# Performance work log

Hardware: AMD Instinct MI355X
Metric: run time of the kernel (lower is better)

The kernel has to match this reference:

```python
import jax, jax.numpy as jnp
import numpy as np

N_NODE = 200000
EMB = 64
N_EDGES = 2000000
LAYERS = 3
EPS_NORM = 1e-12


def setup_inputs() -> dict:
    key = jax.random.key(0)
    ks = jax.random.split(key, 13)
    d = EMB
    return {
        "user_emb": jax.random.normal(ks[0], (N_NODE, d), jnp.float32),
        "W0": jax.random.normal(ks[1], (d, d), jnp.float32) * np.float32(np.sqrt(2.0 / d)),
        "b0": jax.random.normal(ks[2], (1, d), jnp.float32) * 0.1,
        "W1": jax.random.normal(ks[3], (d, d), jnp.float32) * np.float32(np.sqrt(2.0 / d)),
        "b1": jax.random.normal(ks[4], (1, d), jnp.float32) * 0.1,
        "att": jax.random.normal(ks[5], (1, d), jnp.float32) * 0.1,
        "att_m": jax.random.normal(ks[6], (d, d), jnp.float32) * np.float32(np.sqrt(2.0 / d)),
        "item_rows": jax.random.randint(ks[7], (N_EDGES,), 0, N_NODE, jnp.int32),
        "item_cols": jax.random.randint(ks[8], (N_EDGES,), 0, N_NODE, jnp.int32),
        "item_vals": jax.random.uniform(ks[9], (N_EDGES,), jnp.float32),
        "user_rows": jax.random.randint(ks[10], (N_EDGES,), 0, N_NODE, jnp.int32),
        "user_cols": jax.random.randint(ks[11], (N_EDGES,), 0, N_NODE, jnp.int32),
        "user_vals": jax.random.uniform(ks[12], (N_EDGES,), jnp.float32),
    }


def _spmm(rows, cols, vals, x):
    # y[i] = sum_{edges (i,j)} vals * x[j]   (torch.sparse.mm equivalent)
    gathered = vals[:, None] * x[cols]  # [E, d]
    return jax.ops.segment_sum(gathered, rows, num_segments=N_NODE)


def _l2norm_rows(x):
    # F.normalize(x, p=2, dim=1)
    n = jnp.sqrt(jnp.sum(x * x, axis=1, keepdims=True))
    return x / jnp.maximum(n, EPS_NORM)


def _self_gating(em, W, b):
    return em * jax.nn.sigmoid(em @ W + b)


def _propagate(rows, cols, vals, u):
    acc = u
    for _ in range(LAYERS):
        u = _spmm(rows, cols, vals, u)
        acc = acc + _l2norm_rows(u)
    return acc


def reference(user_emb, W0, b0, W1, b1, att, att_m,
              item_rows, item_cols, item_vals,
              user_rows, user_cols, user_vals):
    u_c2 = _self_gating(user_emb, W0, b0)
    u_c3 = _self_gating(user_emb, W1, b1)
    e2 = _propagate(item_rows, item_cols, item_vals, u_c2)  # [N, d]
    e3 = _propagate(user_rows, user_cols, user_vals, u_c3)  # [N, d]
    # channel attention: per-node scalar score for each channel
    w2 = jnp.sum(att * (e2 @ att_m), axis=1)  # [N]
    w3 = jnp.sum(att * (e3 @ att_m), axis=1)  # [N]
    score = jax.nn.softmax(jnp.stack([w2, w3], axis=1), axis=-1)  # [N, 2]
    mixed = score[:, 0:1] * e2 + score[:, 1:2] * e3  # [N, d]
    return mixed, score
```

## Files before the change

kernel.cpp:

```cpp
#include <hip/hip_runtime.h>

#define N_NODE 200000
#define EMB 64
#define N_EDGES 2000000
#define NROWS_TOTAL (2 * N_NODE)
#define TOT_E (2 * N_EDGES)

#define BSHIFT 9
#define BROWS 512
#define NBUCK ((NROWS_TOTAL + BROWS - 1) / BROWS)
#define NB 1024
#define CHUNK ((TOT_E + NB - 1) / NB)
#define SCAN_N (NBUCK * NB)
#define MAXH 6144

typedef unsigned short bfu;
typedef __attribute__((ext_vector_type(8))) short bf16x8;
typedef __attribute__((ext_vector_type(4))) float f32x4;

__device__ __forceinline__ float bf2f(bfu u) { return __uint_as_float(((unsigned)u) << 16); }
__device__ __forceinline__ bfu f2bf(float f) {
    unsigned b = __float_as_uint(f);
    return (bfu)((b + 0x7FFF + ((b >> 16) & 1)) >> 16);
}
__device__ __forceinline__ unsigned packcv(int col, float v) {
    int q = (int)(v * 16384.0f + 0.5f);
    q = q < 0 ? 0 : (q > 16383 ? 16383 : q);
    return ((unsigned)col << 14) | (unsigned)q;
}

__global__ void gate_kernel(const float* __restrict__ emb,
                            const float* __restrict__ W,
                            const float* __restrict__ b,
                            bfu* __restrict__ out, int n) {
    int t = threadIdx.x;
    int w = t >> 6, lane = t & 63;
    int l16 = lane & 15, kg = lane >> 4;
    bf16x8 Bf[2][4];
#pragma unroll
    for (int kb = 0; kb < 2; ++kb)
#pragma unroll
        for (int nt = 0; nt < 4; ++nt) {
            bf16x8 f;
#pragma unroll
            for (int e = 0; e < 8; ++e)
                f[e] = (short)f2bf(W[(kb * 32 + kg * 8 + e) * 64 + nt * 16 + l16]);
            Bf[kb][nt] = f;
        }
    float bias[4];
#pragma unroll
    for (int nt = 0; nt < 4; ++nt) bias[nt] = b[nt * 16 + l16];
    const float4* e4 = (const float4*)emb;
#pragma unroll 1
    for (int it = 0; it < 4; ++it) {
        int tile = blockIdx.x * 16 + w * 4 + it;
        if (tile * 16 >= n) break;
        int arow = tile * 16 + l16;
        size_t ab = (size_t)arow * 16 + kg * 2;
        float4 a0 = e4[ab], a1 = e4[ab + 1];
        float4 a2 = e4[ab + 8], a3 = e4[ab + 9];
        bf16x8 A0, A1;
        A0[0] = (short)f2bf(a0.x); A0[1] = (short)f2bf(a0.y);
        A0[2] = (short)f2bf(a0.z); A0[3] = (short)f2bf(a0.w);
        A0[4] = (short)f2bf(a1.x); A0[5] = (short)f2bf(a1.y);
        A0[6] = (short)f2bf(a1.z); A0[7] = (short)f2bf(a1.w);
        A1[0] = (short)f2bf(a2.x); A1[1] = (short)f2bf(a2.y);
        A1[2] = (short)f2bf(a2.z); A1[3] = (short)f2bf(a2.w);
        A1[4] = (short)f2bf(a3.x); A1[5] = (short)f2bf(a3.y);
        A1[6] = (short)f2bf(a3.z); A1[7] = (short)f2bf(a3.w);
        f32x4 acc[4];
#pragma unroll
        for (int nt = 0; nt < 4; ++nt) {
            acc[nt] = (f32x4){0.f, 0.f, 0.f, 0.f};
            acc[nt] = __builtin_amdgcn_mfma_f32_16x16x32_bf16(A0, Bf[0][nt], acc[nt], 0, 0, 0);
            acc[nt] = __builtin_amdgcn_mfma_f32_16x16x32_bf16(A1, Bf[1][nt], acc[nt], 0, 0, 0);
        }
#pragma unroll
        for (int nt = 0; nt < 4; ++nt) {
#pragma unroll
            for (int r = 0; r < 4; ++r) {
                int orow = tile * 16 + kg * 4 + r;
                int col = nt * 16 + l16;
                float s = acc[nt][r] + bias[nt];
                float g = 1.0f / (1.0f + __expf(-s));
                float xv = emb[(size_t)orow * 64 + col];
                out[(size_t)orow * 64 + col] = f2bf(xv * g);
            }
        }
    }
}

__global__ void binA_kernel(const int* __restrict__ item_rows,
                            const int* __restrict__ user_rows,
                            int* __restrict__ bc) {
    __shared__ int h[NBUCK];
    int t = threadIdx.x, blk = blockIdx.x;
    for (int k = t; k < NBUCK; k += 256) h[k] = 0;
    __syncthreads();
    int lo = blk * CHUNK, hi = min(lo + CHUNK, TOT_E);
    for (int i = lo + t; i < hi; i += 256) {
        int g = (i < N_EDGES) ? item_rows[i] : (N_NODE + user_rows[i - N_EDGES]);
        atomicAdd(&h[g >> BSHIFT], 1);
    }
    __syncthreads();
    for (int k = t; k < NBUCK; k += 256) bc[k * NB + blk] = h[k];
}

__global__ void scan1_kernel(const int* __restrict__ bc, int* __restrict__ bsumP,
                             int* __restrict__ btot) {
    int b = blockIdx.x, t = threadIdx.x;
    int base = b * NB + t * 4;
    int sR = 0, sP = 0;
#pragma unroll
    for (int k = 0; k < 4; ++k) {
        int c = bc[base + k];
        sR += c;
        sP += (c + 7) & ~7;
    }
#pragma unroll
    for (int off = 32; off; off >>= 1) {
        sR += __shfl_xor(sR, off);
        sP += __shfl_xor(sP, off);
    }
    __shared__ int wsR[4], wsP[4];
    int lane = t & 63, w = t >> 6;
    if (lane == 0) { wsR[w] = sR; wsP[w] = sP; }
    __syncthreads();
    if (t == 0) {
        btot[b] = wsR[0] + wsR[1] + wsR[2] + wsR[3];
        bsumP[b] = wsP[0] + wsP[1] + wsP[2] + wsP[3];
    }
}

__global__ void scan2_kernel(const int* __restrict__ bsumP, const int* __restrict__ btot,
                             int* __restrict__ boffP, int* __restrict__ bbase) {
    __shared__ int sh[1024];
    int t = threadIdx.x;
    int vP = (t < NBUCK) ? bsumP[t] : 0;
    sh[t] = vP;
    __syncthreads();
    for (int off = 1; off < 1024; off <<= 1) {
        int u = (t >= off) ? sh[t - off] : 0;
        __syncthreads();
        sh[t] += u;
        __syncthreads();
    }
    if (t < NBUCK) boffP[t] = sh[t] - vP;
    if (t == 1023) boffP[NBUCK] = sh[1023];
    __syncthreads();
    int vR = (t < NBUCK) ? btot[t] : 0;
    sh[t] = vR;
    __syncthreads();
    for (int off = 1; off < 1024; off <<= 1) {
        int u = (t >= off) ? sh[t - off] : 0;
        __syncthreads();
        sh[t] += u;
        __syncthreads();
    }
    if (t < NBUCK) bbase[t] = sh[t] - vR;
}

__global__ void scan3_kernel(const int* __restrict__ bc, const int* __restrict__ boffP,
                             int* __restrict__ soffP) {
    int b = blockIdx.x, t = threadIdx.x;
    int lane = t & 63, w = t >> 6;
    int base = b * NB + t * 4;
    int p[4];
#pragma unroll
    for (int k = 0; k < 4; ++k) p[k] = (bc[base + k] + 7) & ~7;
    int e1 = p[0], e2 = p[0] + p[1], e3 = p[0] + p[1] + p[2];
    int tsum = e3 + p[3];
    int incl = tsum;
#pragma unroll
    for (int off = 1; off < 64; off <<= 1) {
        int u = __shfl_up(incl, off);
        if (lane >= off) incl += u;
    }
    int excl = incl - tsum;
    __shared__ int wsum[4];
    if (lane == 63) wsum[w] = incl;
    __syncthreads();
    int woff = 0;
    for (int k = 0; k < 4; ++k) if (k < w) woff += wsum[k];
    int g = boffP[b] + woff + excl;
    soffP[base + 0] = g;
    soffP[base + 1] = g + e1;
    soffP[base + 2] = g + e2;
    soffP[base + 3] = g + e3;
}

__global__ void binB_kernel(const int* __restrict__ item_rows, const int* __restrict__ item_cols,
                            const float* __restrict__ item_vals,
                            const int* __restrict__ user_rows, const int* __restrict__ user_cols,
                            const float* __restrict__ user_vals,
                            const int* __restrict__ bc, const int* __restrict__ soffP,
                            int2* __restrict__ staged) {
    __shared__ int2 ebuf[CHUNK];
    __shared__ unsigned short sbk[CHUNK];
    __shared__ int lbase[NBUCK + 1];
    __shared__ int lcur[NBUCK];
    __shared__ int gb[NBUCK];
    __shared__ int wsum[4];
    int t = threadIdx.x, blk = blockIdx.x;
    for (int k = t; k < NBUCK; k += 256) gb[k] = soffP[k * NB + blk];
    {
        int i0 = t * 4;
        int p0 = (i0 < NBUCK) ? bc[i0 * NB + blk] : 0;
        int p1 = (i0 + 1 < NBUCK) ? bc[(i0 + 1) * NB + blk] : 0;
        int p2 = (i0 + 2 < NBUCK) ? bc[(i0 + 2) * NB + blk] : 0;
        int p3 = (i0 + 3 < NBUCK) ? bc[(i0 + 3) * NB + blk] : 0;
        int tsum = p0 + p1 + p2 + p3;
        int lane = t & 63, w = t >> 6;
        int incl = tsum;
#pragma unroll
        for (int off = 1; off < 64; off <<= 1) {
            int u = __shfl_up(incl, off);
            if (lane >= off) incl += u;
        }
        if (lane == 63) wsum[w] = incl;
        __syncthreads();
        int woff = 0;
        for (int k = 0; k < w; ++k) woff += wsum[k];
        int excl = woff + incl - tsum;
        if (i0 < NBUCK) { lbase[i0] = excl; lcur[i0] = excl; }
        if (i0 + 1 < NBUCK) { lbase[i0 + 1] = excl + p0; lcur[i0 + 1] = excl + p0; }
        if (i0 + 2 < NBUCK) { lbase[i0 + 2] = excl + p0 + p1; lcur[i0 + 2] = excl + p0 + p1; }
        if (i0 + 3 < NBUCK) { lbase[i0 + 3] = excl + p0 + p1 + p2; lcur[i0 + 3] = excl + p0 + p1 + p2; }
        if (t == 255) lbase[NBUCK] = excl + tsum;
    }
    __syncthreads();
    int lo = blk * CHUNK, hi = min(lo + CHUNK, TOT_E);
    int cnt = hi - lo;
    for (int i = lo + t; i < hi; i += 256) {
        int g, c; float v;
        if (i < N_EDGES) { g = item_rows[i]; c = item_cols[i]; v = item_vals[i]; }
        else { int j = i - N_EDGES; g = N_NODE + user_rows[j]; c = user_cols[j]; v = user_vals[j]; }
        int bk = g >> BSHIFT;
        int s = atomicAdd(&lcur[bk], 1);
        ebuf[s] = make_int2(((g & (BROWS - 1)) << 18) | c, __float_as_int(v));
        sbk[s] = (unsigned short)bk;
    }
    __syncthreads();
    for (int j = t; j < cnt; j += 256) {
        int k = sbk[j];
        staged[gb[k] + (j - lbase[k])] = ebuf[j];
    }
    for (int k = t; k < NBUCK; k += 256) {
        int c = lbase[k + 1] - lbase[k];
        int s = gb[k] + c, e = gb[k] + ((c + 7) & ~7);
        for (int q = s; q < e; ++q) staged[q] = make_int2(-1, 0);
    }
}

__global__ void finalize_kernel(const int2* __restrict__ staged, const int* __restrict__ boffP,
                                const int* __restrict__ bbase,
                                int* __restrict__ row_ptr, unsigned* __restrict__ ecv) {
    __shared__ int hist[BROWS];
    __shared__ int start[BROWS + 1];
    __shared__ int2 ebuf[MAXH];
    __shared__ int wsum[4];
    int b = blockIdx.x, t = threadIdx.x;
    int base = boffP[b], end = boffP[b + 1];
    int ebase = bbase[b];
    hist[t * 2] = 0; hist[t * 2 + 1] = 0;
    __syncthreads();
    for (int k = base + t; k < end; k += 256) {
        int gx = staged[k].x;
        if (gx >= 0) atomicAdd(&hist[gx >> 18], 1);
    }
    __syncthreads();
    int i0 = t * 2;
    int c0 = hist[i0], c1 = hist[i0 + 1];
    int tsum = c0 + c1;
    int lane = t & 63, w = t >> 6;
    int incl = tsum;
#pragma unroll
    for (int off = 1; off < 64; off <<= 1) {
        int u = __shfl_up(incl, off);
        if (lane >= off) incl += u;
    }
    if (lane == 63) wsum[w] = incl;
    __syncthreads();
    int woff = 0;
    for (int k = 0; k < w; ++k) woff += wsum[k];
    int excl = woff + incl - tsum;
    start[i0] = excl; start[i0 + 1] = excl + c0;
    if (t == 255) start[BROWS] = excl + tsum;
    __syncthreads();
    int tot = start[BROWS];
#pragma unroll
    for (int q = 0; q < 2; ++q) {
        int r = i0 + q;
        int g = (b << BSHIFT) + r;
        if (g < NROWS_TOTAL) row_ptr[g] = ebase + start[r];
    }
    if (b == 0 && t == 0) row_ptr[NROWS_TOTAL] = TOT_E;
    if (tot <= MAXH) {
        hist[i0] = start[i0]; hist[i0 + 1] = start[i0 + 1];
        __syncthreads();
        for (int k = base + t; k < end; k += 256) {
            int2 p = staged[k];
            if (p.x < 0) continue;
            int l = atomicAdd(&hist[p.x >> 18], 1);
            ebuf[l] = make_int2(p.x & 0x3FFFF, p.y);
        }
        __syncthreads();
        for (int j = t; j < tot; j += 256) {
            int2 q = ebuf[j];
            ecv[ebase + j] = packcv(q.x, __int_as_float(q.y));
        }
    } else {
        hist[i0] = ebase + start[i0]; hist[i0 + 1] = ebase + start[i0 + 1];
        __syncthreads();
        for (int k = base + t; k < end; k += 256) {
            int2 p = staged[k];
            if (p.x < 0) continue;
            int pos = atomicAdd(&hist[p.x >> 18], 1);
            ecv[pos] = packcv(p.x & 0x3FFFF, __int_as_float(p.y));
        }
    }
}

__global__ void spmm_y(const int* __restrict__ row_ptr, const unsigned* __restrict__ ecv,
                       const bfu* __restrict__ x,
                       bfu* __restrict__ y, float* __restrict__ rinv, int n) {
    int t = threadIdx.x;
    int lane = t & 63;
    int sub = lane >> 4;
    int l16 = lane & 15;
    int i = blockIdx.x * 16 + (t >> 6) * 4 + sub;
    if (i >= n) return;
    int s = row_ptr[i], e = row_ptr[i + 1];
    const ushort4* x4 = (const ushort4*)x;
    float4 a = make_float4(0.f, 0.f, 0.f, 0.f);
    int gbase = sub * 16;
    for (int base = s; base < e; base += 16) {
        int idx = base + l16;
        unsigned pl = 0;
        if (idx < e) pl = ecv[idx];
        int cnt = min(16, e - base);
        int cnt4 = (cnt + 3) & ~3;
        for (int k = 0; k < cnt4; k += 4) {
#pragma unroll
            for (int u = 0; u < 4; ++u) {
                unsigned p = (unsigned)__shfl((int)pl, gbase + k + u);
                int c = p >> 14;
                float v = (float)(p & 16383u) * (1.0f / 16384.0f);
                ushort4 xv = x4[(size_t)c * 16 + l16];
                a.x += v * bf2f(xv.x); a.y += v * bf2f(xv.y);
                a.z += v * bf2f(xv.z); a.w += v * bf2f(xv.w);
            }
        }
    }
    size_t o4 = (size_t)i * 16 + l16;
    ushort4 bv;
    bv.x = f2bf(a.x); bv.y = f2bf(a.y); bv.z = f2bf(a.z); bv.w = f2bf(a.w);
    ((ushort4*)y)[o4] = bv;
    float sq = a.x * a.x + a.y * a.y + a.z * a.z + a.w * a.w;
#pragma unroll
    for (int off = 8; off; off >>= 1) sq += __shfl_xor(sq, off);
    if (l16 == 0) rinv[i] = 1.0f / fmaxf(sqrtf(sq), 1e-12f);
}

__global__ void spmm_sum(const int* __restrict__ row_ptr, const unsigned* __restrict__ ecv,
                         const bfu* __restrict__ x ,
                         const bfu* __restrict__ u0, const bfu* __restrict__ y1,
                         const float* __restrict__ r1, const float* __restrict__ r2,
                         float* __restrict__ mixed, int n) {
    int t = threadIdx.x;
    int lane = t & 63;
    int sub = lane >> 4;
    int l16 = lane & 15;
    int i = blockIdx.x * 16 + (t >> 6) * 4 + sub;
    if (i >= n) return;
    int s = row_ptr[i], e = row_ptr[i + 1];
    const ushort4* x4 = (const ushort4*)x;
    float4 a = make_float4(0.f, 0.f, 0.f, 0.f);
    int gbase = sub * 16;
    for (int base = s; base < e; base += 16) {
        int idx = base + l16;
        unsigned pl = 0;
        if (idx < e) pl = ecv[idx];
        int cnt = min(16, e - base);
        int cnt4 = (cnt + 3) & ~3;
        for (int k = 0; k < cnt4; k += 4) {
#pragma unroll
            for (int u = 0; u < 4; ++u) {
                unsigned p = (unsigned)__shfl((int)pl, gbase + k + u);
                int c = p >> 14;
                float v = (float)(p & 16383u) * (1.0f / 16384.0f);
                ushort4 xv = x4[(size_t)c * 16 + l16];
                a.x += v * bf2f(xv.x); a.y += v * bf2f(xv.y);
                a.z += v * bf2f(xv.z); a.w += v * bf2f(xv.w);
            }
        }
    }
    float sq = a.x * a.x + a.y * a.y + a.z * a.z + a.w * a.w;
#pragma unroll
    for (int off = 8; off; off >>= 1) sq += __shfl_xor(sq, off);
    float r3 = 1.0f / fmaxf(sqrtf(sq), 1e-12f);
    size_t o4 = (size_t)i * 16 + l16;
    float a1 = r1[i], a2 = r2[i];
    ushort4 b0 = ((const ushort4*)u0)[o4];
    ushort4 b1 = ((const ushort4*)y1)[o4];
    ushort4 b2 = ((const ushort4*)x)[o4];
    float4 o;
    o.x = bf2f(b0.x) + a1 * bf2f(b1.x) + a2 * bf2f(b2.x) + r3 * a.x;
    o.y = bf2f(b0.y) + a1 * bf2f(b1.y) + a2 * bf2f(b2.y) + r3 * a.y;
    o.z = bf2f(b0.z) + a1 * bf2f(b1.z) + a2 * bf2f(b2.z) + r3 * a.z;
    o.w = bf2f(b0.w) + a1 * bf2f(b1.w) + a2 * bf2f(b2.w) + r3 * a.w;
    ((float4*)mixed)[o4] = o;
}

__global__ void spmm_mix(const int* __restrict__ row_ptr, const unsigned* __restrict__ ecv,
                         const bfu* __restrict__ x ,
                         const bfu* __restrict__ u0, const bfu* __restrict__ y1,
                         const float* __restrict__ r1, const float* __restrict__ r2,
                         float* __restrict__ mixed, const float* __restrict__ vvec,
                         float* __restrict__ score, int n) {
    int t = threadIdx.x;
    int lane = t & 63;
    int sub = lane >> 4;
    int l16 = lane & 15;
    int i = blockIdx.x * 16 + (t >> 6) * 4 + sub;
    if (i >= n) return;
    int s = row_ptr[i], e = row_ptr[i + 1];
    const ushort4* x4 = (const ushort4*)x;
    float4 a = make_float4(0.f, 0.f, 0.f, 0.f);
    int gbase = sub * 16;
    for (int base = s; base < e; base += 16) {
        int idx = base + l16;
        unsigned pl = 0;
        if (idx < e) pl = ecv[idx];
        int cnt = min(16, e - base);
        int cnt4 = (cnt + 3) & ~3;
        for (int k = 0; k < cnt4; k += 4) {
#pragma unroll
            for (int u = 0; u < 4; ++u) {
                unsigned p = (unsigned)__shfl((int)pl, gbase + k + u);
                int c = p >> 14;
                float v = (float)(p & 16383u) * (1.0f / 16384.0f);
                ushort4 xv = x4[(size_t)c * 16 + l16];
                a.x += v * bf2f(xv.x); a.y += v * bf2f(xv.y);
                a.z += v * bf2f(xv.z); a.w += v * bf2f(xv.w);
            }
        }
    }
    float sq = a.x * a.x + a.y * a.y + a.z * a.z + a.w * a.w;
#pragma unroll
    for (int off = 8; off; off >>= 1) sq += __shfl_xor(sq, off);
    float r3 = 1.0f / fmaxf(sqrtf(sq), 1e-12f);
    size_t o4 = (size_t)i * 16 + l16;
    float a1 = r1[i], a2s = r2[i];
    ushort4 b0 = ((const ushort4*)u0)[o4];
    ushort4 b1 = ((const ushort4*)y1)[o4];
    ushort4 b2 = ((const ushort4*)x)[o4];
    float4 a3;
    a3.x = bf2f(b0.x) + a1 * bf2f(b1.x) + a2s * bf2f(b2.x) + r3 * a.x;
    a3.y = bf2f(b0.y) + a1 * bf2f(b1.y) + a2s * bf2f(b2.y) + r3 * a.y;
    a3.z = bf2f(b0.z) + a1 * bf2f(b1.z) + a2s * bf2f(b2.z) + r3 * a.z;
    a3.w = bf2f(b0.w) + a1 * bf2f(b1.w) + a2s * bf2f(b2.w) + r3 * a.w;
    float4 a2 = ((float4*)mixed)[o4];
    float4 vv = ((const float4*)vvec)[l16];
    float w2 = a2.x * vv.x + a2.y * vv.y + a2.z * vv.z + a2.w * vv.w;
    float w3 = a3.x * vv.x + a3.y * vv.y + a3.z * vv.z + a3.w * vv.w;
#pragma unroll
    for (int off = 8; off; off >>= 1) {
        w2 += __shfl_xor(w2, off);
        w3 += __shfl_xor(w3, off);
    }
    float m = fmaxf(w2, w3);
    float x2 = __expf(w2 - m), x3 = __expf(w3 - m);
    float inv = 1.0f / (x2 + x3);
    float s2 = x2 * inv, s3 = x3 * inv;
    float4 o;
    o.x = s2 * a2.x + s3 * a3.x; o.y = s2 * a2.y + s3 * a3.y;
    o.z = s2 * a2.z + s3 * a3.z; o.w = s2 * a2.w + s3 * a3.w;
    ((float4*)mixed)[o4] = o;
    if (l16 == 0) { score[(size_t)i * 2] = s2; score[(size_t)i * 2 + 1] = s3; }
}

__global__ void vvec_kernel(const float* __restrict__ att_m, const float* __restrict__ att,
                            float* __restrict__ v) {
    int k = threadIdx.x;
    float s = 0.0f;
    for (int j = 0; j < 64; ++j) s += att_m[k * 64 + j] * att[j];
    v[k] = s;
}

extern "C" void kernel_launch(void* const* d_in, const int* in_sizes, int n_in,
                              void* d_out, int out_size, void* d_ws, size_t ws_size,
                              hipStream_t stream) {
    const float* user_emb = (const float*)d_in[0];
    const float* W0 = (const float*)d_in[1];
    const float* b0 = (const float*)d_in[2];
    const float* W1 = (const float*)d_in[3];
    const float* b1 = (const float*)d_in[4];
    const float* att = (const float*)d_in[5];
    const float* att_m = (const float*)d_in[6];
    const int* item_rows = (const int*)d_in[7];
    const int* item_cols = (const int*)d_in[8];
    const float* item_vals = (const float*)d_in[9];
    const int* user_rows = (const int*)d_in[10];
    const int* user_cols = (const int*)d_in[11];
    const float* user_vals = (const float*)d_in[12];

    float* out = (float*)d_out;
    float* mixed = out;
    float* score = out + (size_t)N_NODE * 64;

    char* w = (char*)d_ws;
    bfu* u0 = (bfu*)w;         w += (size_t)N_NODE * 64 * 2;
    bfu* y1 = (bfu*)w;         w += (size_t)N_NODE * 64 * 2;
    bfu* y2 = (bfu*)w;         w += (size_t)N_NODE * 64 * 2;
    float* rv1 = (float*)w;    w += (size_t)N_NODE * 4;
    float* rv2 = (float*)w;    w += (size_t)N_NODE * 4;
    int* row_ptr = (int*)w;    w += ((size_t)NROWS_TOTAL + 64) * 4;
    unsigned* ecv = (unsigned*)w; w += (size_t)TOT_E * 4;
    float* vvec = (float*)w;   w += 256;
    int* bc = (int*)w;         w += (size_t)SCAN_N * 4;
    int* soffP = (int*)w;      w += (size_t)SCAN_N * 4;
    int* bsumP = (int*)w;      w += (NBUCK + 8) * 4;
    int* btot = (int*)w;       w += (NBUCK + 8) * 4;
    int* boffP = (int*)w;      w += (NBUCK + 8) * 4;
    int* bbase = (int*)w;      w += (NBUCK + 8) * 4;
    int2* staged = (int2*)u0;

    const int NB16 = (N_NODE + 15) / 16;
    const int GATE_B = (N_NODE / 16 + 15) / 16;
    const int* rp_item = row_ptr;
    const int* rp_user = row_ptr + N_NODE;

    binA_kernel<<<NB, 256, 0, stream>>>(item_rows, user_rows, bc);
    scan1_kernel<<<NBUCK, 256, 0, stream>>>(bc, bsumP, btot);
    scan2_kernel<<<1, 1024, 0, stream>>>(bsumP, btot, boffP, bbase);
    scan3_kernel<<<NBUCK, 256, 0, stream>>>(bc, boffP, soffP);
    binB_kernel<<<NB, 256, 0, stream>>>(item_rows, item_cols, item_vals,
                                        user_rows, user_cols, user_vals, bc, soffP, staged);
    finalize_kernel<<<NBUCK, 256, 0, stream>>>(staged, boffP, bbase, row_ptr, ecv);
    vvec_kernel<<<1, 64, 0, stream>>>(att_m, att, vvec);

    gate_kernel<<<GATE_B, 256, 0, stream>>>(user_emb, W0, b0, u0, N_NODE);
    spmm_y<<<NB16, 256, 0, stream>>>(rp_item, ecv, u0, y1, rv1, N_NODE);
    spmm_y<<<NB16, 256, 0, stream>>>(rp_item, ecv, y1, y2, rv2, N_NODE);
    spmm_sum<<<NB16, 256, 0, stream>>>(rp_item, ecv, y2, u0, y1, rv1, rv2, mixed, N_NODE);

    gate_kernel<<<GATE_B, 256, 0, stream>>>(user_emb, W1, b1, u0, N_NODE);
    spmm_y<<<NB16, 256, 0, stream>>>(rp_user, ecv, u0, y1, rv1, N_NODE);
    spmm_y<<<NB16, 256, 0, stream>>>(rp_user, ecv, y1, y2, rv2, N_NODE);
    spmm_mix<<<NB16, 256, 0, stream>>>(rp_user, ecv, y2, u0, y1, rv1, rv2,
                                       mixed, vvec, score, N_NODE);
}
```

Before: 438.3 us.

## Batch both propagation channels into single launches over stacked node rows

Doubles the workspace buffers so the item and user channels are stored side by side. The two gating passes and the per-layer SpMMs for both channels each run as one launch over all rows, and the final layer of both channels is merged with the attention mix into a single kernel. This cuts the launch count, avoids writing then re-reading the intermediate mixed output, and gives each SpMM launch twice the rows to fill the GPU. In exchange the workspace footprint grows and the final kernel does two gathers per thread, which raises register pressure.

```diff
diff --git a/kernel.cpp b/kernel.cpp
--- a/kernel.cpp
+++ b/kernel.cpp
@@ -13,6 +13,7 @@
 #define CHUNK ((TOT_E + NB - 1) / NB)
 #define SCAN_N (NBUCK * NB)
 #define MAXH 6144
+#define GATE_B ((N_NODE / 16 + 15) / 16)
 
 typedef unsigned short bfu;
 typedef __attribute__((ext_vector_type(8))) short bf16x8;
@@ -29,10 +30,16 @@
     return ((unsigned)col << 14) | (unsigned)q;
 }
 
-__global__ void gate_kernel(const float* __restrict__ emb,
-                            const float* __restrict__ W,
-                            const float* __restrict__ b,
-                            bfu* __restrict__ out, int n) {
+__global__ void gate2_kernel(const float* __restrict__ emb,
+                             const float* __restrict__ W0, const float* __restrict__ b0,
+                             const float* __restrict__ W1, const float* __restrict__ b1,
+                             bfu* __restrict__ out) {
+    int blk = blockIdx.x;
+    int half = (blk >= GATE_B) ? 1 : 0;
+    const float* W = half ? W1 : W0;
+    const float* b = half ? b1 : b0;
+    bfu* o = out + (size_t)half * N_NODE * 64;
+    int bblk = blk - half * GATE_B;
     int t = threadIdx.x;
     int w = t >> 6, lane = t & 63;
     int l16 = lane & 15, kg = lane >> 4;
@@ -53,8 +60,8 @@
     const float4* e4 = (const float4*)emb;
 #pragma unroll 1
     for (int it = 0; it < 4; ++it) {
-        int tile = blockIdx.x * 16 + w * 4 + it;
-        if (tile * 16 >= n) break;
+        int tile = bblk * 16 + w * 4 + it;
+        if (tile * 16 >= N_NODE) break;
         int arow = tile * 16 + l16;
         size_t ab = (size_t)arow * 16 + kg * 2;
         float4 a0 = e4[ab], a1 = e4[ab + 1];
@@ -84,7 +91,7 @@
                 float s = acc[nt][r] + bias[nt];
                 float g = 1.0f / (1.0f + __expf(-s));
                 float xv = emb[(size_t)orow * 64 + col];
-                out[(size_t)orow * 64 + col] = f2bf(xv * g);
+                o[(size_t)orow * 64 + col] = f2bf(xv * g);
             }
         }
     }
@@ -323,13 +330,14 @@
 
 __global__ void spmm_y(const int* __restrict__ row_ptr, const unsigned* __restrict__ ecv,
                        const bfu* __restrict__ x,
-                       bfu* __restrict__ y, float* __restrict__ rinv, int n) {
+                       bfu* __restrict__ y, float* __restrict__ rinv) {
     int t = threadIdx.x;
     int lane = t & 63;
     int sub = lane >> 4;
     int l16 = lane & 15;
     int i = blockIdx.x * 16 + (t >> 6) * 4 + sub;
-    if (i >= n) return;
+    if (i >= NROWS_TOTAL) return;
+    size_t off16 = (i >= N_NODE) ? (size_t)N_NODE * 16 : 0;
     int s = row_ptr[i], e = row_ptr[i + 1];
     const ushort4* x4 = (const ushort4*)x;
     float4 a = make_float4(0.f, 0.f, 0.f, 0.f);
@@ -346,7 +354,7 @@
                 unsigned p = (unsigned)__shfl((int)pl, gbase + k + u);
                 int c = p >> 14;
                 float v = (float)(p & 16383u) * (1.0f / 16384.0f);
-                ushort4 xv = x4[(size_t)c * 16 + l16];
+                ushort4 xv = x4[(size_t)c * 16 + off16 + l16];
                 a.x += v * bf2f(xv.x); a.y += v * bf2f(xv.y);
                 a.z += v * bf2f(xv.z); a.w += v * bf2f(xv.w);
             }
@@ -362,108 +370,92 @@
     if (l16 == 0) rinv[i] = 1.0f / fmaxf(sqrtf(sq), 1e-12f);
 }
 
-__global__ void spmm_sum(const int* __restrict__ row_ptr, const unsigned* __restrict__ ecv,
-                         const bfu* __restrict__ x ,
+__global__ void spmm_fin(const int* __restrict__ row_ptr, const unsigned* __restrict__ ecv,
+                         const bfu* __restrict__ y2 ,
                          const bfu* __restrict__ u0, const bfu* __restrict__ y1,
-                         const float* __restrict__ r1, const float* __restrict__ r2,
-                         float* __restrict__ mixed, int n) {
+                         const float* __restrict__ rv1, const float* __restrict__ rv2,
+                         float* __restrict__ mixed, const float* __restrict__ vvec,
+                         float* __restrict__ score) {
     int t = threadIdx.x;
     int lane = t & 63;
     int sub = lane >> 4;
     int l16 = lane & 15;
     int i = blockIdx.x * 16 + (t >> 6) * 4 + sub;
-    if (i >= n) return;
-    int s = row_ptr[i], e = row_ptr[i + 1];
-    const ushort4* x4 = (const ushort4*)x;
-    float4 a = make_float4(0.f, 0.f, 0.f, 0.f);
+    if (i >= N_NODE) return;
+    const ushort4* x4 = (const ushort4*)y2;
     int gbase = sub * 16;
-    for (int base = s; base < e; base += 16) {
-        int idx = base + l16;
-        unsigned pl = 0;
-        if (idx < e) pl = ecv[idx];
-        int cnt = min(16, e - base);
-        int cnt4 = (cnt + 3) & ~3;
-        for (int k = 0; k < cnt4; k += 4) {
-#pragma unroll
-            for (int u = 0; u < 4; ++u) {
-                unsigned p = (unsigned)__shfl((int)pl, gbase + k + u);
-                int c = p >> 14;
-                float v = (float)(p & 16383u) * (1.0f / 16384.0f);
-                ushort4 xv = x4[(size_t)c * 16 + l16];
-                a.x += v * bf2f(xv.x); a.y += v * bf2f(xv.y);
-                a.z += v * bf2f(xv.z); a.w += v * bf2f(xv.w);
+    float4 a2v = make_float4(0.f, 0.f, 0.f, 0.f);
+    {
+        int s = row_ptr[i], e = row_ptr[i + 1];
+        for (int base = s; base < e; base += 16) {
+            int idx = base + l16;
+            unsigned pl = 0;
+            if (idx < e) pl = ecv[idx];
+            int cnt = min(16, e - base);
+            int cnt4 = (cnt + 3) & ~3;
+            for (int k = 0; k < cnt4; k += 4) {
+#pragma unroll
+                for (int u = 0; u < 4; ++u) {
+                    unsigned p = (unsigned)__shfl((int)pl, gbase + k + u);
+                    int c = p >> 14;
+                    float v = (float)(p & 16383u) * (1.0f / 16384.0f);
+                    ushort4 xv = x4[(size_t)c * 16 + l16];
+                    a2v.x += v * bf2f(xv.x); a2v.y += v * bf2f(xv.y);
+                    a2v.z += v * bf2f(xv.z); a2v.w += v * bf2f(xv.w);
+                }
             }
         }
     }
-    float sq = a.x * a.x + a.y * a.y + a.z * a.z + a.w * a.w;
-#pragma unroll
-    for (int off = 8; off; off >>= 1) sq += __shfl_xor(sq, off);
-    float r3 = 1.0f / fmaxf(sqrtf(sq), 1e-12f);
-    size_t o4 = (size_t)i * 16 + l16;
-    float a1 = r1[i], a2 = r2[i];
-    ushort4 b0 = ((const ushort4*)u0)[o4];
-    ushort4 b1 = ((const ushort4*)y1)[o4];
-    ushort4 b2 = ((const ushort4*)x)[o4];
-    float4 o;
-    o.x = bf2f(b0.x) + a1 * bf2f(b1.x) + a2 * bf2f(b2.x) + r3 * a.x;
-    o.y = bf2f(b0.y) + a1 * bf2f(b1.y) + a2 * bf2f(b2.y) + r3 * a.y;
-    o.z = bf2f(b0.z) + a1 * bf2f(b1.z) + a2 * bf2f(b2.z) + r3 * a.z;
-    o.w = bf2f(b0.w) + a1 * bf2f(b1.w) + a2 * bf2f(b2.w) + r3 * a.w;
-    ((float4*)mixed)[o4] = o;
-}
-
-__global__ void spmm_mix(const int* __restrict__ row_ptr, const unsigned* __restrict__ ecv,
-                         const bfu* __restrict__ x ,
-                         const bfu* __restrict__ u0, const bfu* __restrict__ y1,
-                         const float* __restrict__ r1, const float* __restrict__ r2,
-                         float* __restrict__ mixed, const float* __restrict__ vvec,
-                         float* __restrict__ score, int n) {
-    int t = threadIdx.x;
-    int lane = t & 63;
-    int sub = lane >> 4;
-    int l16 = lane & 15;
-    int i = blockIdx.x * 16 + (t >> 6) * 4 + sub;
-    if (i >= n) return;
-    int s = row_ptr[i], e = row_ptr[i + 1];
-    const ushort4* x4 = (const ushort4*)x;
-    float4 a = make_float4(0.f, 0.f, 0.f, 0.f);
-    int gbase = sub * 16;
-    for (int base = s; base < e; base += 16) {
-        int idx = base + l16;
-        unsigned pl = 0;
-        if (idx < e) pl = ecv[idx];
-        int cnt = min(16, e - base);
-        int cnt4 = (cnt + 3) & ~3;
-        for (int k = 0; k < cnt4; k += 4) {
-#pragma unroll
-            for (int u = 0; u < 4; ++u) {
-                unsigned p = (unsigned)__shfl((int)pl, gbase + k + u);
-                int c = p >> 14;
-                float v = (float)(p & 16383u) * (1.0f / 16384.0f);
-                ushort4 xv = x4[(size_t)c * 16 + l16];
-                a.x += v * bf2f(xv.x); a.y += v * bf2f(xv.y);
-                a.z += v * bf2f(xv.z); a.w += v * bf2f(xv.w);
+    float4 a3v = make_float4(0.f, 0.f, 0.f, 0.f);
+    {
+        int s = row_ptr[N_NODE + i], e = row_ptr[N_NODE + i + 1];
+        for (int base = s; base < e; base += 16) {
+            int idx = base + l16;
+            unsigned pl = 0;
+            if (idx < e) pl = ecv[idx];
+            int cnt = min(16, e - base);
+            int cnt4 = (cnt + 3) & ~3;
+            for (int k = 0; k < cnt4; k += 4) {
+#pragma unroll
+                for (int u = 0; u < 4; ++u) {
+                    unsigned p = (unsigned)__shfl((int)pl, gbase + k + u);
+                    int c = p >> 14;
+                    float v = (float)(p & 16383u) * (1.0f / 16384.0f);
+                    ushort4 xv = x4[(size_t)c * 16 + (size_t)N_NODE * 16 + l16];
+                    a3v.x += v * bf2f(xv.x); a3v.y += v * bf2f(xv.y);
+                    a3v.z += v * bf2f(xv.z); a3v.w += v * bf2f(xv.w);
+                }
             }
         }
     }
-    float sq = a.x * a.x + a.y * a.y + a.z * a.z + a.w * a.w;
-#pragma unroll
-    for (int off = 8; off; off >>= 1) sq += __shfl_xor(sq, off);
-    float r3 = 1.0f / fmaxf(sqrtf(sq), 1e-12f);
-    size_t o4 = (size_t)i * 16 + l16;
-    float a1 = r1[i], a2s = r2[i];
-    ushort4 b0 = ((const ushort4*)u0)[o4];
-    ushort4 b1 = ((const ushort4*)y1)[o4];
-    ushort4 b2 = ((const ushort4*)x)[o4];
-    float4 a3;
-    a3.x = bf2f(b0.x) + a1 * bf2f(b1.x) + a2s * bf2f(b2.x) + r3 * a.x;
-    a3.y = bf2f(b0.y) + a1 * bf2f(b1.y) + a2s * bf2f(b2.y) + r3 * a.y;
-    a3.z = bf2f(b0.z) + a1 * bf2f(b1.z) + a2s * bf2f(b2.z) + r3 * a.z;
-    a3.w = bf2f(b0.w) + a1 * bf2f(b1.w) + a2s * bf2f(b2.w) + r3 * a.w;
-    float4 a2 = ((float4*)mixed)[o4];
+    float sq2 = a2v.x * a2v.x + a2v.y * a2v.y + a2v.z * a2v.z + a2v.w * a2v.w;
+    float sq3 = a3v.x * a3v.x + a3v.y * a3v.y + a3v.z * a3v.z + a3v.w * a3v.w;
+#pragma unroll
+    for (int off = 8; off; off >>= 1) {
+        sq2 += __shfl_xor(sq2, off);
+        sq3 += __shfl_xor(sq3, off);
+    }
+    float r3a = 1.0f / fmaxf(sqrtf(sq2), 1e-12f);
+    float r3b = 1.0f / fmaxf(sqrtf(sq3), 1e-12f);
+    size_t oA = (size_t)i * 16 + l16;
+    size_t oB = (size_t)(N_NODE + i) * 16 + l16;
+    float a1A = rv1[i], a2A = rv2[i];
+    float a1B = rv1[N_NODE + i], a2B = rv2[N_NODE + i];
+    ushort4 uA = ((const ushort4*)u0)[oA], uB = ((const ushort4*)u0)[oB];
+    ushort4 y1A = ((const ushort4*)y1)[oA], y1B = ((const ushort4*)y1)[oB];
+    ushort4 y2A = ((const ushort4*)y2)[oA], y2B = ((const ushort4*)y2)[oB];
+    float4 e2, e3;
+    e2.x = bf2f(uA.x) + a1A * bf2f(y1A.x) + a2A * bf2f(y2A.x) + r3a * a2v.x;
+    e2.y = bf2f(uA.y) + a1A * bf2f(y1A.y) + a2A * bf2f(y2A.y) + r3a * a2v.y;
+    e2.z = bf2f(uA.z) + a1A * bf2f(y1A.z) + a2A * bf2f(y2A.z) + r3a * a2v.z;
+    e2.w = bf2f(uA.w) + a1A * bf2f(y1A.w) + a2A * bf2f(y2A.w) + r3a * a2v.w;
+    e3.x = bf2f(uB.x) + a1B * bf2f(y1B.x) + a2B * bf2f(y2B.x) + r3b * a3v.x;
+    e3.y = bf2f(uB.y) + a1B * bf2f(y1B.y) + a2B * bf2f(y2B.y) + r3b * a3v.y;
+    e3.z = bf2f(uB.z) + a1B * bf2f(y1B.z) + a2B * bf2f(y2B.z) + r3b * a3v.z;
+    e3.w = bf2f(uB.w) + a1B * bf2f(y1B.w) + a2B * bf2f(y2B.w) + r3b * a3v.w;
     float4 vv = ((const float4*)vvec)[l16];
-    float w2 = a2.x * vv.x + a2.y * vv.y + a2.z * vv.z + a2.w * vv.w;
-    float w3 = a3.x * vv.x + a3.y * vv.y + a3.z * vv.z + a3.w * vv.w;
+    float w2 = e2.x * vv.x + e2.y * vv.y + e2.z * vv.z + e2.w * vv.w;
+    float w3 = e3.x * vv.x + e3.y * vv.y + e3.z * vv.z + e3.w * vv.w;
 #pragma unroll
     for (int off = 8; off; off >>= 1) {
         w2 += __shfl_xor(w2, off);
@@ -474,9 +466,9 @@
     float inv = 1.0f / (x2 + x3);
     float s2 = x2 * inv, s3 = x3 * inv;
     float4 o;
-    o.x = s2 * a2.x + s3 * a3.x; o.y = s2 * a2.y + s3 * a3.y;
-    o.z = s2 * a2.z + s3 * a3.z; o.w = s2 * a2.w + s3 * a3.w;
-    ((float4*)mixed)[o4] = o;
+    o.x = s2 * e2.x + s3 * e3.x; o.y = s2 * e2.y + s3 * e3.y;
+    o.z = s2 * e2.z + s3 * e3.z; o.w = s2 * e2.w + s3 * e3.w;
+    ((float4*)mixed)[oA] = o;
     if (l16 == 0) { score[(size_t)i * 2] = s2; score[(size_t)i * 2 + 1] = s3; }
 }
 
@@ -510,11 +502,11 @@
     float* score = out + (size_t)N_NODE * 64;
 
     char* w = (char*)d_ws;
-    bfu* u0 = (bfu*)w;         w += (size_t)N_NODE * 64 * 2;
-    bfu* y1 = (bfu*)w;         w += (size_t)N_NODE * 64 * 2;
-    bfu* y2 = (bfu*)w;         w += (size_t)N_NODE * 64 * 2;
-    float* rv1 = (float*)w;    w += (size_t)N_NODE * 4;
-    float* rv2 = (float*)w;    w += (size_t)N_NODE * 4;
+    bfu* u0 = (bfu*)w;         w += (size_t)NROWS_TOTAL * 64 * 2;
+    bfu* y1 = (bfu*)w;         w += (size_t)NROWS_TOTAL * 64 * 2;
+    bfu* y2 = (bfu*)w;         w += (size_t)NROWS_TOTAL * 64 * 2;
+    float* rv1 = (float*)w;    w += (size_t)NROWS_TOTAL * 4;
+    float* rv2 = (float*)w;    w += (size_t)NROWS_TOTAL * 4;
     int* row_ptr = (int*)w;    w += ((size_t)NROWS_TOTAL + 64) * 4;
     unsigned* ecv = (unsigned*)w; w += (size_t)TOT_E * 4;
     float* vvec = (float*)w;   w += 256;
@@ -526,10 +518,8 @@
     int* bbase = (int*)w;      w += (NBUCK + 8) * 4;
     int2* staged = (int2*)u0;
 
+    const int NBALL = (NROWS_TOTAL + 15) / 16;
     const int NB16 = (N_NODE + 15) / 16;
-    const int GATE_B = (N_NODE / 16 + 15) / 16;
-    const int* rp_item = row_ptr;
-    const int* rp_user = row_ptr + N_NODE;
 
     binA_kernel<<<NB, 256, 0, stream>>>(item_rows, user_rows, bc);
     scan1_kernel<<<NBUCK, 256, 0, stream>>>(bc, bsumP, btot);
@@ -540,14 +530,9 @@
     finalize_kernel<<<NBUCK, 256, 0, stream>>>(staged, boffP, bbase, row_ptr, ecv);
     vvec_kernel<<<1, 64, 0, stream>>>(att_m, att, vvec);
 
-    gate_kernel<<<GATE_B, 256, 0, stream>>>(user_emb, W0, b0, u0, N_NODE);
-    spmm_y<<<NB16, 256, 0, stream>>>(rp_item, ecv, u0, y1, rv1, N_NODE);
-    spmm_y<<<NB16, 256, 0, stream>>>(rp_item, ecv, y1, y2, rv2, N_NODE);
-    spmm_sum<<<NB16, 256, 0, stream>>>(rp_item, ecv, y2, u0, y1, rv1, rv2, mixed, N_NODE);
-
-    gate_kernel<<<GATE_B, 256, 0, stream>>>(user_emb, W1, b1, u0, N_NODE);
-    spmm_y<<<NB16, 256, 0, stream>>>(rp_user, ecv, u0, y1, rv1, N_NODE);
-    spmm_y<<<NB16, 256, 0, stream>>>(rp_user, ecv, y1, y2, rv2, N_NODE);
-    spmm_mix<<<NB16, 256, 0, stream>>>(rp_user, ecv, y2, u0, y1, rv1, rv2,
-                                       mixed, vvec, score, N_NODE);
-}
+    gate2_kernel<<<2 * GATE_B, 256, 0, stream>>>(user_emb, W0, b0, W1, b1, u0);
+    spmm_y<<<NBALL, 256, 0, stream>>>(row_ptr, ecv, u0, y1, rv1);
+    spmm_y<<<NBALL, 256, 0, stream>>>(row_ptr, ecv, y1, y2, rv2);
+    spmm_fin<<<NB16, 256, 0, stream>>>(row_ptr, ecv, y2, u0, y1, rv1, rv2,
+                                       mixed, vvec, score);
+}
```

New measurement: 419.2 us. -4.4%, faster.
